# Kernel optimization log

Measured on AMD Instinct MI355X. Metric: run time of the kernel, lower is better.

## Reference

```python
import jax, jax.numpy as jnp
import numpy as np

B, S, H, NH = 2, 2048, 128, 8  # batch, seq, num_hidden (= per-head dim), num_heads
LN_EPS = 1e-5


def _ln(x, g, b):
    m = jnp.mean(x, axis=-1, keepdims=True)
    v = jnp.var(x, axis=-1, keepdims=True)
    return (x - m) / jnp.sqrt(v + LN_EPS) * g + b


def setup_inputs() -> dict:
    key = jax.random.key(0)
    ks = jax.random.split(key, 18)
    sc = 0.02
    d = {}
    d["x"] = jax.random.normal(ks[0], (B, S, H), jnp.float32)
    # per-head full-dim projections, stacked over heads: [NH, H, H] (in->out layout)
    d["Wq"] = jax.random.normal(ks[1], (NH, H, H), jnp.float32) * sc
    d["bq"] = jax.random.normal(ks[2], (NH, H), jnp.float32) * sc
    d["Wk"] = jax.random.normal(ks[3], (NH, H, H), jnp.float32) * sc
    d["bk"] = jax.random.normal(ks[4], (NH, H), jnp.float32) * sc
    d["Wv"] = jax.random.normal(ks[5], (NH, H, H), jnp.float32) * sc
    d["bv"] = jax.random.normal(ks[6], (NH, H), jnp.float32) * sc
    d["Wo"] = jax.random.normal(ks[7], (NH * H, H), jnp.float32) * sc
    d["bo"] = jax.random.normal(ks[8], (H,), jnp.float32) * sc
    # conv1x1 FFN == pointwise linears: [H, 2H] and [2H, H]
    d["W1"] = jax.random.normal(ks[9], (H, 2 * H), jnp.float32) * sc
    d["b1"] = jax.random.normal(ks[10], (2 * H,), jnp.float32) * sc
    d["W2"] = jax.random.normal(ks[11], (2 * H, H), jnp.float32) * sc
    d["b2"] = jax.random.normal(ks[12], (H,), jnp.float32) * sc
    d["g1"] = jnp.ones((H,), jnp.float32)
    d["beta1"] = jnp.zeros((H,), jnp.float32)
    d["g2"] = jnp.ones((H,), jnp.float32)
    d["beta2"] = jnp.zeros((H,), jnp.float32)
    return d


def reference(x, Wq, bq, Wk, bk, Wv, bv, Wo, bo, W1, b1, W2, b2, g1, beta1, g2, beta2):
    # Multi-head attention: each head uses the FULL embed dim (faithful to source).
    Q = jnp.einsum('bsd,hde->bhse', x, Wq) + bq[None, :, None, :]
    K = jnp.einsum('bsd,hde->bhse', x, Wk) + bk[None, :, None, :]
    V = jnp.einsum('bsd,hde->bhse', x, Wv) + bv[None, :, None, :]
    scores = jnp.einsum('bhse,bhte->bhst', Q, K) / jnp.sqrt(jnp.float32(H))
    A = jax.nn.softmax(scores, axis=-1)          # [B, NH, S, S]
    o = jnp.einsum('bhst,bhte->bhse', A, V)      # [B, NH, S, H]
    o = o.transpose(0, 2, 1, 3).reshape(x.shape[0], x.shape[1], NH * H)  # concat heads
    y = o @ Wo + bo                               # W_O projection
    y = _ln(y, g1, beta1)                         # norm1 (no residual around attn, per source)
    f = jax.nn.relu(jax.nn.relu(y @ W1 + b1) @ W2 + b2)  # conv1x1 -> relu -> conv1x1 -> relu
    y = _ln(y + f, g2, beta2)                     # residual + norm2
    return y
```

## Files before the change

kernel.cpp:

```cpp
#include <hip/hip_runtime.h>
#include <math.h>

#define Bq  2
#define Sq  2048
#define Hq  128
#define NHq 8

typedef __attribute__((ext_vector_type(8))) short bf16x8;
typedef __attribute__((ext_vector_type(4))) float f32x4;
typedef __attribute__((ext_vector_type(16))) float f32x16;
typedef __attribute__((ext_vector_type(4))) unsigned short ushort4_t;
typedef __attribute__((ext_vector_type(4))) unsigned int uint4v;
typedef __attribute__((ext_vector_type(2))) unsigned long long u64x2;
typedef unsigned short ushort_t;
typedef unsigned int uint_t;
typedef unsigned long long u64;

__device__ inline ushort_t f2bf(float f) {
    union { float f; uint_t u; } c; c.f = f;
    uint_t u = c.u + 0x7FFFu + ((c.u >> 16) & 1u);
    return (ushort_t)(u >> 16);
}
__device__ inline float bf2f(ushort_t u) {
    union { uint_t u; float f; } c; c.u = ((uint_t)u) << 16;
    return c.f;
}

__device__ inline float exp2_fast(float x) {
    float r;
    asm("v_exp_f32 %0, %1" : "=v"(r) : "v"(x));
    return r;
}

__device__ inline uint_t cvtpk_bf16(float lo, float hi) {
    uint_t r;
    asm("v_cvt_pk_bf16_f32 %0, %1, %2" : "=v"(r) : "v"(lo), "v"(hi));
    return r;
}
__device__ inline void pswap32(uint_t &a, uint_t &b) {
    asm("v_permlane32_swap_b32 %0, %1" : "+v"(a), "+v"(b));
}

#define GLOAD16(gsrc, ldst) \
    __builtin_amdgcn_global_load_lds( \
        (const __attribute__((address_space(1))) unsigned int*)(const void*)(gsrc), \
        (__attribute__((address_space(3))) unsigned int*)(ldst), 16, 0, 0)

__global__ __launch_bounds__(256) void tw_kernel(
    const float* __restrict__ Wq, const float* __restrict__ Wk, const float* __restrict__ Wv,
    const float* __restrict__ Wo, const float* __restrict__ W1, const float* __restrict__ W2,
    const float* __restrict__ x,
    ushort_t* __restrict__ Wt_all, ushort_t* __restrict__ Wot,
    ushort_t* __restrict__ W1t, ushort_t* __restrict__ W2t, ushort_t* __restrict__ xb)
{
    const int z = blockIdx.y;
    const int t = threadIdx.x;

    if (z == 27) {
        const int r0 = blockIdx.x << 5;
        #pragma unroll
        for (int i = 0; i < 2; ++i) {
            const int c = t + i * 256;
            const int row = r0 + (c >> 4), j = (c & 15) * 8;
            const float* xp = x + (size_t)row * 128 + j;
            const float4 a = *(const float4*)xp;
            const float4 b = *(const float4*)(xp + 4);
            bf16x8 v;
            v[0]=f2bf(a.x); v[1]=f2bf(a.y); v[2]=f2bf(a.z); v[3]=f2bf(a.w);
            v[4]=f2bf(b.x); v[5]=f2bf(b.y); v[6]=f2bf(b.z); v[7]=f2bf(b.w);
            *(bf16x8*)&xb[(size_t)row * 128 + j] = v;
        }
        return;
    }

    const float* src; ushort_t* dst; int R, C;
    if (z < 24) { const int h = z & 7;
        src = (z < 8 ? Wq : z < 16 ? Wk : Wv) + h * 16384;
        dst = Wt_all + z * 16384; R = 128; C = 128;
    } else if (z == 24) { src = Wo; dst = Wot; R = 1024; C = 128; }
    else if (z == 25)   { src = W1; dst = W1t; R = 128;  C = 256; }
    else                { src = W2; dst = W2t; R = 256;  C = 128; }

    const int tpc = C >> 5;
    if ((int)blockIdx.x >= (R >> 5) * tpc) return;
    const int r0 = (blockIdx.x / tpc) << 5;
    const int c0 = (blockIdx.x % tpc) << 5;

    __shared__ float ls[32][33];
    const int lr = t >> 5, lc = t & 31;
    #pragma unroll
    for (int i = 0; i < 4; ++i)
        ls[lr + i * 8][lc] = src[(size_t)(r0 + lr + i * 8) * C + c0 + lc];
    __syncthreads();
    const int wc = t >> 3, wr0 = (t & 7) << 2;
    ushort4_t o4;
    o4[0] = f2bf(ls[wr0 + 0][wc]); o4[1] = f2bf(ls[wr0 + 1][wc]);
    o4[2] = f2bf(ls[wr0 + 2][wc]); o4[3] = f2bf(ls[wr0 + 3][wc]);
    *(ushort4_t*)&dst[(size_t)(c0 + wc) * R + r0 + wr0] = o4;
}

__global__ __launch_bounds__(256) void qkv_gemm(
    const ushort_t* __restrict__ xb, const ushort_t* __restrict__ Wt_all,
    const float* __restrict__ bq, const float* __restrict__ bk, const float* __restrict__ bv,
    ushort_t* __restrict__ Qb, ushort_t* __restrict__ Kb, ushort_t* __restrict__ Vb)
{
    __shared__ ushort_t As[64 * 128];
    __shared__ ushort_t Bs[128 * 128];
    const int tid = threadIdx.x;
    const int w = tid >> 6, l = tid & 63, lg = l >> 4, ln = l & 15;
    const int m0 = blockIdx.x << 6;

    #pragma unroll
    for (int i = 0; i < 4; ++i) {
        const int seg = w * 4 + i;
        const int row = seg * 4 + (l >> 4);
        const int j = (l & 15) ^ (row & 15);
        GLOAD16(xb + (size_t)(m0 + row) * 128 + j * 8, &As[seg * 512]);
    }

    bf16x8 af[4];

    #pragma unroll
    for (int half = 0; half < 2; ++half) {
        const int z = blockIdx.y + half * 12;
        const ushort_t* Wz = Wt_all + (size_t)z * 16384;
        #pragma unroll
        for (int i = 0; i < 8; ++i) {
            const int seg = w * 8 + i;
            const int row = seg * 4 + (l >> 4);
            const int j = (l & 15) ^ (row & 15);
            GLOAD16(Wz + row * 128 + j * 8, &Bs[seg * 512]);
        }
        __syncthreads();

        if (half == 0) {
            #pragma unroll
            for (int kc = 0; kc < 4; ++kc)
                af[kc] = *(const bf16x8*)&As[(w * 16 + ln) * 128 + (((kc * 4 + lg) ^ ln) << 3)];
        }

        f32x4 acc[8];
        #pragma unroll
        for (int nt = 0; nt < 8; ++nt) acc[nt] = (f32x4){0.f,0.f,0.f,0.f};
        #pragma unroll
        for (int nt = 0; nt < 8; ++nt)
            #pragma unroll
            for (int kc = 0; kc < 4; ++kc) {
                const bf16x8 bn = *(const bf16x8*)&Bs[(nt * 16 + ln) * 128 + (((kc * 4 + lg) ^ ln) << 3)];
                acc[nt] = __builtin_amdgcn_mfma_f32_16x16x32_bf16(af[kc], bn, acc[nt], 0, 0, 0);
            }

        const float* bias = (z < 8 ? bq : z < 16 ? bk : bv) + (z & 7) * 128;
        ushort_t* outp = (z < 8 ? Qb : z < 16 ? Kb : Vb);
        const float scale = z < 8 ? (0.08838834764831845f * 1.4426950408889634f) : 1.0f;
        const int h = z & 7;
        #pragma unroll
        for (int nt = 0; nt < 8; ++nt) {
            const float bb = bias[nt * 16 + ln];
            #pragma unroll
            for (int j2 = 0; j2 < 4; ++j2) {
                const int r = m0 + w * 16 + lg * 4 + j2;
                const int b = r >> 11, s = r & 2047;
                outp[((size_t)((b << 3) + h) * 2048 + s) * 128 + nt * 16 + ln] =
                    f2bf((acc[nt][j2] + bb) * scale);
            }
        }
        __syncthreads();
    }
}

__global__ __launch_bounds__(256, 2) void attn_kernel(
    const ushort_t* __restrict__ Q, const ushort_t* __restrict__ K,
    const ushort_t* __restrict__ V, ushort_t* __restrict__ Opart,
    float2* __restrict__ ml)
{
    __shared__ ushort_t sh[32768];
    ushort_t* Vt = sh + 16384;

    const int tid = threadIdx.x;
    const int w = tid >> 6, l = tid & 63;
    const int ln5 = l & 31, h5 = l >> 5;

    const int id  = blockIdx.x;
    const int id2 = (id & 7) * 64 + (id >> 3);
    const int s   = id2 >> 8;
    const int bh  = (id2 >> 4) & 15;
    const int q0  = (id2 & 15) << 7;
    const int kv0 = s << 10;

    const size_t base = (size_t)bh * Sq * Hq;
    const ushort_t* Qp = Q + base;
    const ushort_t* Kp = K + base + (size_t)kv0 * Hq;
    const ushort_t* Vp = V + base + (size_t)kv0 * Hq;

    bf16x8 qf[8];
    {
        const ushort_t* qrow = Qp + (size_t)(q0 + w * 32 + ln5) * Hq;
        #pragma unroll
        for (int kc = 0; kc < 8; ++kc)
            qf[kc] = *(const bf16x8*)(qrow + kc * 16 + h5 * 8);
    }

    const int kv2 = (tid & 31) * 2;
    const int d8  = (tid >> 5) * 8;

    f32x16 po[4];
    #pragma unroll
    for (int dt = 0; dt < 4; ++dt)
        #pragma unroll
        for (int r = 0; r < 16; ++r) po[dt][r] = 0.f;
    float m_ = -1e30f, l_ = 0.f;

    #pragma unroll
    for (int i = 0; i < 4; ++i) {
        const int seg = w * 4 + i;
        const int row = seg * 4 + (l >> 4);
        const int j = (l & 15) ^ (row & 15);
        GLOAD16(Kp + (size_t)row * Hq + j * 8, &sh[seg * 512]);
    }
    bf16x8 va0 = *(const bf16x8*)(Vp + (size_t)kv2 * Hq + d8);
    bf16x8 va1 = *(const bf16x8*)(Vp + (size_t)(kv2 + 1) * Hq + d8);
    bf16x8 vb0 = *(const bf16x8*)(Vp + (size_t)kv2 * Hq + d8 + 64);
    bf16x8 vb1 = *(const bf16x8*)(Vp + (size_t)(kv2 + 1) * Hq + d8 + 64);
    __syncthreads();
    #pragma unroll
    for (int jj = 0; jj < 8; ++jj) {
        const int r1 = d8 + jj, r2 = d8 + 64 + jj;
        *(uint_t*)&Vt[r1 * 128 + ((((kv2 >> 3) ^ (r1 & 15))) << 3) + (kv2 & 7)] =
            (uint_t)(ushort_t)va0[jj] | ((uint_t)(ushort_t)va1[jj] << 16);
        *(uint_t*)&Vt[r2 * 128 + ((((kv2 >> 3) ^ (r2 & 15))) << 3) + (kv2 & 7)] =
            (uint_t)(ushort_t)vb0[jj] | ((uint_t)(ushort_t)vb1[jj] << 16);
    }
    __syncthreads();

    const int NT = 1024 / 64;
    for (int t = 0; t < NT; ++t) {
        const int buf = t & 1;
        const ushort_t* Ksb = sh + buf * 8192;

        f32x16 st[2];
        #pragma unroll
        for (int mt = 0; mt < 2; ++mt)
            #pragma unroll
            for (int r = 0; r < 16; ++r) st[mt][r] = 0.f;

        __builtin_amdgcn_s_setprio(1);
        #pragma unroll
        for (int kc = 0; kc < 8; ++kc) {
            #pragma unroll
            for (int mt = 0; mt < 2; ++mt) {
                const int row = mt * 32 + ln5;
                const int slot = (kc * 2 + h5) ^ (row & 15);
                const bf16x8 ka = *(const bf16x8*)&Ksb[row * 128 + (slot << 3)];
                st[mt] = __builtin_amdgcn_mfma_f32_32x32x16_bf16(ka, qf[kc], st[mt], 0, 0, 0);
            }
        }
        __builtin_amdgcn_s_setprio(0);

        if (t + 1 < NT) {
            const int k0n = (t + 1) * 64;
            #pragma unroll
            for (int i = 0; i < 4; ++i) {
                const int seg = w * 4 + i;
                const int row = seg * 4 + (l >> 4);
                const int j = (l & 15) ^ (row & 15);
                GLOAD16(Kp + (size_t)(k0n + row) * Hq + j * 8, &sh[(buf ^ 1) * 8192 + seg * 512]);
            }
            va0 = *(const bf16x8*)(Vp + (size_t)(k0n + kv2) * Hq + d8);
            va1 = *(const bf16x8*)(Vp + (size_t)(k0n + kv2 + 1) * Hq + d8);
            vb0 = *(const bf16x8*)(Vp + (size_t)(k0n + kv2) * Hq + d8 + 64);
            vb1 = *(const bf16x8*)(Vp + (size_t)(k0n + kv2 + 1) * Hq + d8 + 64);
        }

        float mxv[16];
        #pragma unroll
        for (int r = 0; r < 16; ++r) mxv[r] = fmaxf(st[0][r], st[1][r]);
        #pragma unroll
        for (int sd = 8; sd >= 1; sd >>= 1)
            #pragma unroll
            for (int i = 0; i < sd; ++i) mxv[i] = fmaxf(mxv[i], mxv[i + sd]);
        float mx = mxv[0];
        mx = fmaxf(mx, __shfl_xor(mx, 32));

        const bool anyup = __any(mx > m_ + 8.0f);
        float sc = 1.0f;
        if (anyup) {
            const float mn = fmaxf(m_, mx);
            sc = exp2_fast(m_ - mn);
            m_ = mn;
        }

        float pe[32];
        #pragma unroll
        for (int mt = 0; mt < 2; ++mt)
            #pragma unroll
            for (int r = 0; r < 16; ++r)
                pe[mt * 16 + r] = exp2_fast(st[mt][r] - m_);

        float sv[16];
        #pragma unroll
        for (int r = 0; r < 16; ++r) sv[r] = pe[r] + pe[16 + r];
        #pragma unroll
        for (int sd = 8; sd >= 1; sd >>= 1)
            #pragma unroll
            for (int i = 0; i < sd; ++i) sv[i] += sv[i + sd];
        float rs = sv[0];
        rs += __shfl_xor(rs, 32);
        l_ = l_ * sc + rs;

        bf16x8 pb[4];
        #pragma unroll
        for (int ks = 0; ks < 4; ++ks) {
            const int o = (ks >> 1) * 16 + (ks & 1) * 8;
            uint_t wA = cvtpk_bf16(pe[o + 0], pe[o + 1]);
            uint_t wB = cvtpk_bf16(pe[o + 4], pe[o + 5]);
            pswap32(wA, wB);
            uint_t wC = cvtpk_bf16(pe[o + 2], pe[o + 3]);
            uint_t wD = cvtpk_bf16(pe[o + 6], pe[o + 7]);
            pswap32(wC, wD);
            uint4v wv; wv[0] = wA; wv[1] = wC; wv[2] = wB; wv[3] = wD;
            pb[ks] = __builtin_bit_cast(bf16x8, wv);
        }

        if (anyup) {
            #pragma unroll
            for (int dt = 0; dt < 4; ++dt)
                #pragma unroll
                for (int r = 0; r < 16; ++r) po[dt][r] *= sc;
        }

        __builtin_amdgcn_s_setprio(1);
        #pragma unroll
        for (int dt = 0; dt < 4; ++dt) {
            #pragma unroll
            for (int ks = 0; ks < 4; ++ks) {
                const int row = dt * 32 + ln5;
                const int slot = (ks * 2 + h5) ^ (row & 15);
                const bf16x8 va = *(const bf16x8*)&Vt[row * 128 + (slot << 3)];
                po[dt] = __builtin_amdgcn_mfma_f32_32x32x16_bf16(va, pb[ks], po[dt], 0, 0, 0);
            }
        }
        __builtin_amdgcn_s_setprio(0);

        __syncthreads();
        if (t + 1 < NT) {
            #pragma unroll
            for (int jj = 0; jj < 8; ++jj) {
                const int r1 = d8 + jj, r2 = d8 + 64 + jj;
                *(uint_t*)&Vt[r1 * 128 + ((((kv2 >> 3) ^ (r1 & 15))) << 3) + (kv2 & 7)] =
                    (uint_t)(ushort_t)va0[jj] | ((uint_t)(ushort_t)va1[jj] << 16);
                *(uint_t*)&Vt[r2 * 128 + ((((kv2 >> 3) ^ (r2 & 15))) << 3) + (kv2 & 7)] =
                    (uint_t)(ushort_t)vb0[jj] | ((uint_t)(ushort_t)vb1[jj] << 16);
            }
        }
        __syncthreads();
    }

    char* shb = (char*)sh;
    char* wb = shb + w * 8448;
    #pragma unroll
    for (int dt = 0; dt < 4; ++dt)
        #pragma unroll
        for (int r = 0; r < 16; r += 2) {
            const int d = dt * 32 + (r & 3) + 8 * (r >> 2) + 4 * h5;
            const uint_t pk = cvtpk_bf16(po[dt][r], po[dt][r + 1]);
            *(uint_t*)(wb + ln5 * 264 + d * 2) = pk;
        }
    const int rid0 = (s * 16 + bh) * 2048 + q0 + w * 32;
    #pragma unroll
    for (int rb = 0; rb < 8; ++rb) {
        const int qr = rb * 4 + (l >> 4);
        const char* rp = wb + qr * 264 + (l & 15) * 16;
        u64x2 vv;
        vv[0] = *(const u64*)rp;
        vv[1] = *(const u64*)(rp + 8);
        *(u64x2*)(Opart + (size_t)(rid0 + qr) * 128 + (l & 15) * 8) = vv;
    }
    if (h5 == 0)
        ml[rid0 + ln5] = make_float2(m_, l_);
}

__global__ __launch_bounds__(256) void wo_ffn_kernel(
    const ushort_t* __restrict__ Opart, const float2* __restrict__ ml,
    const ushort_t* __restrict__ Wot, const float* __restrict__ bo,
    const float* __restrict__ g1, const float* __restrict__ be1,
    const ushort_t* __restrict__ W1t, const float* __restrict__ b1,
    const ushort_t* __restrict__ W2t, const float* __restrict__ b2,
    const float* __restrict__ g2, const float* __restrict__ be2,
    float* __restrict__ out)
{
    __shared__ ushort_t As[32 * 128];
    __shared__ ushort_t Bs[128 * 128];
    __shared__ ushort_t Hs[2][32 * 128];
    __shared__ float ybuf[32 * 132];
    const int tid = threadIdx.x;
    const int w = tid >> 6, l = tid & 63, lg = l >> 4, ln = l & 15;
    const int m0 = blockIdx.x << 5;
    const int rw = (w & 1) * 16;
    const int cw = (w >> 1) * 4;

    f32x4 acc[4];
    #pragma unroll
    for (int nt = 0; nt < 4; ++nt) acc[nt] = (f32x4){0.f,0.f,0.f,0.f};

    for (int ks = 0; ks < 8; ++ks) {
        const int k0 = ks << 7;
        #pragma unroll
        for (int i = 0; i < 2; ++i) {
            const int c = tid + i * 256;
            const int row = c >> 4, j = c & 15;
            const int r = m0 + row, b = r >> 11, q = r & 2047;
            const int prow = ((b << 3) + ks) * 2048 + q;
            const float2 e0 = ml[prow];
            const float2 e1 = ml[32768 + prow];
            const float M = fmaxf(e0.x, e1.x);
            const float w0 = exp2_fast(e0.x - M), w1 = exp2_fast(e1.x - M);
            const float inv = 1.0f / (w0 * e0.y + w1 * e1.y);
            const size_t po_ = (size_t)prow * 128 + j * 8;
            const bf16x8 o0 = *(const bf16x8*)&Opart[po_];
            const bf16x8 o1 = *(const bf16x8*)&Opart[po_ + (size_t)32768 * 128];
            bf16x8 mv;
            #pragma unroll
            for (int jj = 0; jj < 8; ++jj) {
                const float v = (w0 * bf2f((ushort_t)o0[jj]) + w1 * bf2f((ushort_t)o1[jj])) * inv;
                mv[jj] = (short)f2bf(v);
            }
            *(bf16x8*)&As[row * 128 + ((j ^ (row & 15)) << 3)] = mv;
        }
        #pragma unroll
        for (int i = 0; i < 8; ++i) {
            const int seg = w * 8 + i;
            const int row = seg * 4 + (l >> 4);
            const int j = (l & 15) ^ (row & 15);
            GLOAD16(Wot + (size_t)row * 1024 + k0 + j * 8, &Bs[seg * 512]);
        }
        __syncthreads();

        bf16x8 af0[4];
        #pragma unroll
        for (int kc = 0; kc < 4; ++kc)
            af0[kc] = *(const bf16x8*)&As[(rw + ln) * 128 + (((kc * 4 + lg) ^ ln) << 3)];
        #pragma unroll
        for (int nt = 0; nt < 4; ++nt)
            #pragma unroll
            for (int kc = 0; kc < 4; ++kc) {
                const bf16x8 bn = *(const bf16x8*)&Bs[((cw + nt) * 16 + ln) * 128 + (((kc * 4 + lg) ^ ln) << 3)];
                acc[nt] = __builtin_amdgcn_mfma_f32_16x16x32_bf16(af0[kc], bn, acc[nt], 0, 0, 0);
            }
        __syncthreads();
    }

    #pragma unroll
    for (int nt = 0; nt < 4; ++nt) {
        const int col = (cw + nt) * 16 + ln;
        const float bb = bo[col];
        #pragma unroll
        for (int j2 = 0; j2 < 4; ++j2)
            ybuf[(rw + lg * 4 + j2) * 132 + col] = acc[nt][j2] + bb;
    }
    __syncthreads();

    {
        const int row = tid >> 3, sub = tid & 7;
        float vals[16];
        float sm = 0.f, sq = 0.f;
        #pragma unroll
        for (int e = 0; e < 16; ++e) {
            const float v = ybuf[row * 132 + sub * 16 + e];
            vals[e] = v; sm += v; sq += v * v;
        }
        #pragma unroll
        for (int mmk = 1; mmk <= 4; mmk <<= 1) {
            sm += __shfl_xor(sm, mmk);
            sq += __shfl_xor(sq, mmk);
        }
        const float mean = sm * (1.0f / 128.0f);
        const float var  = sq * (1.0f / 128.0f) - mean * mean;
        const float rstd = rsqrtf(var + 1e-5f);
        #pragma unroll
        for (int e = 0; e < 16; e += 2) {
            const int col = sub * 16 + e;
            const float v0 = (vals[e]   - mean) * rstd * g1[col]   + be1[col];
            const float v1 = (vals[e+1] - mean) * rstd * g1[col+1] + be1[col+1];
            ybuf[row * 132 + col]     = v0;
            ybuf[row * 132 + col + 1] = v1;
            const int jch = col >> 3;
            *(uint_t*)&As[row * 128 + ((jch ^ (row & 15)) << 3) + (col & 7)] =
                (uint_t)f2bf(v0) | ((uint_t)f2bf(v1) << 16);
        }
    }
    __syncthreads();

    bf16x8 af[4];
    #pragma unroll
    for (int half = 0; half < 2; ++half) {
        const int n0 = half << 7;
        #pragma unroll
        for (int i = 0; i < 8; ++i) {
            const int seg = w * 8 + i;
            const int row = seg * 4 + (l >> 4);
            const int j = (l & 15) ^ (row & 15);
            GLOAD16(W1t + (size_t)(n0 + row) * 128 + j * 8, &Bs[seg * 512]);
        }
        __syncthreads();

        if (half == 0) {
            #pragma unroll
            for (int kc = 0; kc < 4; ++kc)
                af[kc] = *(const bf16x8*)&As[(rw + ln) * 128 + (((kc * 4 + lg) ^ ln) << 3)];
        }

        f32x4 acc1[4];
        #pragma unroll
        for (int nt = 0; nt < 4; ++nt) acc1[nt] = (f32x4){0.f,0.f,0.f,0.f};
        #pragma unroll
        for (int nt = 0; nt < 4; ++nt)
            #pragma unroll
            for (int kc = 0; kc < 4; ++kc) {
                const bf16x8 bn = *(const bf16x8*)&Bs[((cw + nt) * 16 + ln) * 128 + (((kc * 4 + lg) ^ ln) << 3)];
                acc1[nt] = __builtin_amdgcn_mfma_f32_16x16x32_bf16(af[kc], bn, acc1[nt], 0, 0, 0);
            }

        #pragma unroll
        for (int nt = 0; nt < 4; ++nt) {
            const int colh = (cw + nt) * 16 + ln;
            const float bb = b1[n0 + colh];
            #pragma unroll
            for (int j2 = 0; j2 < 4; ++j2) {
                const int row = rw + lg * 4 + j2;
                const float v = fmaxf(acc1[nt][j2] + bb, 0.f);
                Hs[half][row * 128 + ((((colh >> 3) ^ (row & 15))) << 3) + (colh & 7)] = f2bf(v);
            }
        }
        __syncthreads();
    }

    f32x4 acc2[4];
    #pragma unroll
    for (int nt = 0; nt < 4; ++nt) acc2[nt] = (f32x4){0.f,0.f,0.f,0.f};

    #pragma unroll
    for (int ks = 0; ks < 2; ++ks) {
        const int k0 = ks << 7;
        #pragma unroll
        for (int i = 0; i < 8; ++i) {
            const int seg = w * 8 + i;
            const int row = seg * 4 + (l >> 4);
            const int j = (l & 15) ^ (row & 15);
            GLOAD16(W2t + (size_t)row * 256 + k0 + j * 8, &Bs[seg * 512]);
        }
        __syncthreads();

        bf16x8 af2[4];
        #pragma unroll
        for (int kc = 0; kc < 4; ++kc)
            af2[kc] = *(const bf16x8*)&Hs[ks][(rw + ln) * 128 + (((kc * 4 + lg) ^ ln) << 3)];
        #pragma unroll
        for (int nt = 0; nt < 4; ++nt)
            #pragma unroll
            for (int kc = 0; kc < 4; ++kc) {
                const bf16x8 bn = *(const bf16x8*)&Bs[((cw + nt) * 16 + ln) * 128 + (((kc * 4 + lg) ^ ln) << 3)];
                acc2[nt] = __builtin_amdgcn_mfma_f32_16x16x32_bf16(af2[kc], bn, acc2[nt], 0, 0, 0);
            }
        __syncthreads();
    }

    #pragma unroll
    for (int nt = 0; nt < 4; ++nt) {
        const int col = (cw + nt) * 16 + ln;
        const float bb = b2[col];
        #pragma unroll
        for (int j2 = 0; j2 < 4; ++j2) {
            const int row = rw + lg * 4 + j2;
            const float f = fmaxf(acc2[nt][j2] + bb, 0.f);
            ybuf[row * 132 + col] = f + ybuf[row * 132 + col];
        }
    }
    __syncthreads();

    {
        const int row = tid >> 3, sub = tid & 7;
        float vals[16];
        float sm = 0.f, sq = 0.f;
        #pragma unroll
        for (int e = 0; e < 16; ++e) {
            const float v = ybuf[row * 132 + sub * 16 + e];
            vals[e] = v; sm += v; sq += v * v;
        }
        #pragma unroll
        for (int mmk = 1; mmk <= 4; mmk <<= 1) {
            sm += __shfl_xor(sm, mmk);
            sq += __shfl_xor(sq, mmk);
        }
        const float mean = sm * (1.0f / 128.0f);
        const float var  = sq * (1.0f / 128.0f) - mean * mean;
        const float rstd = rsqrtf(var + 1e-5f);
        float* op = out + (size_t)(m0 + row) * 128 + sub * 16;
        #pragma unroll
        for (int e = 0; e < 16; ++e) {
            const int col = sub * 16 + e;
            op[e] = (vals[e] - mean) * rstd * g2[col] + be2[col];
        }
    }
}

extern "C" void kernel_launch(void* const* d_in, const int* in_sizes, int n_in,
                              void* d_out, int out_size, void* d_ws, size_t ws_size,
                              hipStream_t stream)
{
    const float* x   = (const float*)d_in[0];
    const float* Wq  = (const float*)d_in[1];
    const float* bq  = (const float*)d_in[2];
    const float* Wk  = (const float*)d_in[3];
    const float* bk  = (const float*)d_in[4];
    const float* Wv  = (const float*)d_in[5];
    const float* bv  = (const float*)d_in[6];
    const float* Wo  = (const float*)d_in[7];
    const float* bo  = (const float*)d_in[8];
    const float* W1  = (const float*)d_in[9];
    const float* b1  = (const float*)d_in[10];
    const float* W2  = (const float*)d_in[11];
    const float* b2  = (const float*)d_in[12];
    const float* g1  = (const float*)d_in[13];
    const float* be1 = (const float*)d_in[14];
    const float* g2  = (const float*)d_in[15];
    const float* be2 = (const float*)d_in[16];
    (void)in_sizes; (void)n_in; (void)out_size; (void)ws_size;

    ushort_t* Wt_all = (ushort_t*)d_ws;
    ushort_t* Wot   = Wt_all + 393216;
    ushort_t* W1t   = Wot + 131072;
    ushort_t* W2t   = W1t + 32768;
    ushort_t* xb    = W2t + 32768;
    ushort_t* Qb    = xb + 524288;
    ushort_t* Kb    = Qb + 4194304;
    ushort_t* Vb    = Kb + 4194304;
    ushort_t* Opart = Vb + 4194304;
    float2*   ml    = (float2*)(Opart + 8388608);

    tw_kernel    <<<dim3(128, 28), 256, 0, stream>>>(Wq, Wk, Wv, Wo, W1, W2, x,
                                                     Wt_all, Wot, W1t, W2t, xb);
    qkv_gemm     <<<dim3(64, 12),  256, 0, stream>>>(xb, Wt_all, bq, bk, bv, Qb, Kb, Vb);
    attn_kernel  <<<dim3(512),     256, 0, stream>>>(Qb, Kb, Vb, Opart, ml);
    wo_ffn_kernel<<<dim3(128),     256, 0, stream>>>(Opart, ml, Wot, bo, g1, be1,
                                                     W1t, b1, W2t, b2, g2, be2,
                                                     (float*)d_out);
}
```

Before: 82.60 us.

## Double-buffer Wo GEMM stages to overlap partial merge and loads with MFMA

Doubles the As/Bs shared buffers in the Wo+FFN kernel and prefetches the next K-slice (Wo tile load plus the softmax-partial merge) while computing MFMAs on the current slice. This removes one barrier per iteration and hides global-load and merge latency behind matrix work. It raises LDS usage substantially, which can limit occupancy, and the merge math now competes with MFMA issue within the same waves.

Measured after the change: 82.49 us. No clear change (-0.1%).

```diff
diff --git a/kernel.cpp b/kernel.cpp
--- a/kernel.cpp
+++ b/kernel.cpp
@@ -389,8 +389,8 @@
     const float* __restrict__ g2, const float* __restrict__ be2,
     float* __restrict__ out)
 {
-    __shared__ ushort_t As[32 * 128];
-    __shared__ ushort_t Bs[128 * 128];
+    __shared__ ushort_t As[2][32 * 128];
+    __shared__ ushort_t Bs[2][128 * 128];
     __shared__ ushort_t Hs[2][32 * 128];
     __shared__ float ybuf[32 * 132];
     const int tid = threadIdx.x;
@@ -399,18 +399,13 @@
     const int rw = (w & 1) * 16;
     const int cw = (w >> 1) * 4;
 
-    f32x4 acc[4];
-    #pragma unroll
-    for (int nt = 0; nt < 4; ++nt) acc[nt] = (f32x4){0.f,0.f,0.f,0.f};
-
-    for (int ks = 0; ks < 8; ++ks) {
-        const int k0 = ks << 7;
+    auto mergeA = [&](int kh, int bsel) {
         #pragma unroll
         for (int i = 0; i < 2; ++i) {
             const int c = tid + i * 256;
             const int row = c >> 4, j = c & 15;
-            const int r = m0 + row, b = r >> 11, q = r & 2047;
-            const int prow = ((b << 3) + ks) * 2048 + q;
+            const int r = m0 + row, bb_ = r >> 11, q = r & 2047;
+            const int prow = ((bb_ << 3) + kh) * 2048 + q;
             const float2 e0 = ml[prow];
             const float2 e1 = ml[32768 + prow];
             const float M = fmaxf(e0.x, e1.x);
@@ -425,26 +420,43 @@
                 const float v = (w0 * bf2f((ushort_t)o0[jj]) + w1 * bf2f((ushort_t)o1[jj])) * inv;
                 mv[jj] = (short)f2bf(v);
             }
-            *(bf16x8*)&As[row * 128 + ((j ^ (row & 15)) << 3)] = mv;
-        }
+            *(bf16x8*)&As[bsel][row * 128 + ((j ^ (row & 15)) << 3)] = mv;
+        }
+    };
+    auto stageB = [&](int kh, int bsel) {
         #pragma unroll
         for (int i = 0; i < 8; ++i) {
             const int seg = w * 8 + i;
             const int row = seg * 4 + (l >> 4);
             const int j = (l & 15) ^ (row & 15);
-            GLOAD16(Wot + (size_t)row * 1024 + k0 + j * 8, &Bs[seg * 512]);
-        }
-        __syncthreads();
+            GLOAD16(Wot + (size_t)row * 1024 + (kh << 7) + j * 8, &Bs[bsel][seg * 512]);
+        }
+    };
+
+    f32x4 acc[4];
+    #pragma unroll
+    for (int nt = 0; nt < 4; ++nt) acc[nt] = (f32x4){0.f,0.f,0.f,0.f};
+
+    stageB(0, 0);
+    mergeA(0, 0);
+    __syncthreads();
+
+    for (int ks = 0; ks < 8; ++ks) {
+        const int cur = ks & 1;
+        if (ks + 1 < 8) {
+            stageB(ks + 1, cur ^ 1);
+            mergeA(ks + 1, cur ^ 1);
+        }
 
         bf16x8 af0[4];
         #pragma unroll
         for (int kc = 0; kc < 4; ++kc)
-            af0[kc] = *(const bf16x8*)&As[(rw + ln) * 128 + (((kc * 4 + lg) ^ ln) << 3)];
+            af0[kc] = *(const bf16x8*)&As[cur][(rw + ln) * 128 + (((kc * 4 + lg) ^ ln) << 3)];
         #pragma unroll
         for (int nt = 0; nt < 4; ++nt)
             #pragma unroll
             for (int kc = 0; kc < 4; ++kc) {
-                const bf16x8 bn = *(const bf16x8*)&Bs[((cw + nt) * 16 + ln) * 128 + (((kc * 4 + lg) ^ ln) << 3)];
+                const bf16x8 bn = *(const bf16x8*)&Bs[cur][((cw + nt) * 16 + ln) * 128 + (((kc * 4 + lg) ^ ln) << 3)];
                 acc[nt] = __builtin_amdgcn_mfma_f32_16x16x32_bf16(af0[kc], bn, acc[nt], 0, 0, 0);
             }
         __syncthreads();
@@ -485,7 +497,7 @@
             ybuf[row * 132 + col]     = v0;
             ybuf[row * 132 + col + 1] = v1;
             const int jch = col >> 3;
-            *(uint_t*)&As[row * 128 + ((jch ^ (row & 15)) << 3) + (col & 7)] =
+            *(uint_t*)&As[0][row * 128 + ((jch ^ (row & 15)) << 3) + (col & 7)] =
                 (uint_t)f2bf(v0) | ((uint_t)f2bf(v1) << 16);
         }
     }
@@ -500,14 +512,14 @@
             const int seg = w * 8 + i;
             const int row = seg * 4 + (l >> 4);
             const int j = (l & 15) ^ (row & 15);
-            GLOAD16(W1t + (size_t)(n0 + row) * 128 + j * 8, &Bs[seg * 512]);
+            GLOAD16(W1t + (size_t)(n0 + row) * 128 + j * 8, &Bs[0][seg * 512]);
         }
         __syncthreads();
 
         if (half == 0) {
             #pragma unroll
             for (int kc = 0; kc < 4; ++kc)
-                af[kc] = *(const bf16x8*)&As[(rw + ln) * 128 + (((kc * 4 + lg) ^ ln) << 3)];
+                af[kc] = *(const bf16x8*)&As[0][(rw + ln) * 128 + (((kc * 4 + lg) ^ ln) << 3)];
         }
 
         f32x4 acc1[4];
@@ -517,7 +529,7 @@
         for (int nt = 0; nt < 4; ++nt)
             #pragma unroll
             for (int kc = 0; kc < 4; ++kc) {
-                const bf16x8 bn = *(const bf16x8*)&Bs[((cw + nt) * 16 + ln) * 128 + (((kc * 4 + lg) ^ ln) << 3)];
+                const bf16x8 bn = *(const bf16x8*)&Bs[0][((cw + nt) * 16 + ln) * 128 + (((kc * 4 + lg) ^ ln) << 3)];
                 acc1[nt] = __builtin_amdgcn_mfma_f32_16x16x32_bf16(af[kc], bn, acc1[nt], 0, 0, 0);
             }
 
@@ -547,7 +559,7 @@
             const int seg = w * 8 + i;
             const int row = seg * 4 + (l >> 4);
             const int j = (l & 15) ^ (row & 15);
-            GLOAD16(W2t + (size_t)row * 256 + k0 + j * 8, &Bs[seg * 512]);
+            GLOAD16(W2t + (size_t)row * 256 + k0 + j * 8, &Bs[0][seg * 512]);
         }
         __syncthreads();
 
@@ -559,7 +571,7 @@
         for (int nt = 0; nt < 4; ++nt)
             #pragma unroll
             for (int kc = 0; kc < 4; ++kc) {
-                const bf16x8 bn = *(const bf16x8*)&Bs[((cw + nt) * 16 + ln) * 128 + (((kc * 4 + lg) ^ ln) << 3)];
+                const bf16x8 bn = *(const bf16x8*)&Bs[0][((cw + nt) * 16 + ln) * 128 + (((kc * 4 + lg) ^ ln) << 3)];
                 acc2[nt] = __builtin_amdgcn_mfma_f32_16x16x32_bf16(af2[kc], bn, acc2[nt], 0, 0, 0);
             }
         __syncthreads();
```
